# Kernel optimization log

Hardware: AMD Instinct MI355X
Metric: run time of the kernel (lower is better)

## Reference

```python
import jax, jax.numpy as jnp
import numpy as np

# Reconstructed laminar V1-V2 dynamics (submodule sources were not provided;
# dynamics follow the documented dependency order L4 -> PV -> V2 -> template -> SOM -> L2/3).
N = 36            # n_orientations
H = 128           # v2_hidden_dim
DT_TAU = 0.1      # dt/tau for rate units
DT_TAU_A = 0.02   # dt/tau for adaptation
BETA_A = 0.5      # adaptation strength
W_PV = 1.0        # PV (divisive-ish subtractive) inhibition weight
W_SOM = 0.8       # SOM inhibition weight
FB_GAIN = 0.5     # feedback center-excitation gain
ALPHA = 1.0       # error-signal template subtraction
FB_SCALE = 1.0    # feedback_scale buffer


def _ring_kernel(key, n, scale):
    return scale * jax.random.normal(key, (n, n), dtype=jnp.float32)


def setup_inputs() -> dict:
    key = jax.random.key(0)
    ks = jax.random.split(key, 16)
    B, T = 1024, 512
    D_in = 2 * N + 2  # 74 packed width
    s = 1.0 / np.sqrt(N)
    sh = 1.0 / np.sqrt(D_in + H)
    return {
        "packed_input": jax.random.normal(ks[0], (B, T, D_in), dtype=jnp.float32),
        "W_l4": _ring_kernel(ks[1], N, s),
        "W_l23": _ring_kernel(ks[2], N, s),
        "W_som": _ring_kernel(ks[3], N, s),
        "Wz": sh * jax.random.normal(ks[4], (D_in + H, H), dtype=jnp.float32),
        "Wr": sh * jax.random.normal(ks[5], (D_in + H, H), dtype=jnp.float32),
        "Wh": sh * jax.random.normal(ks[6], (D_in + H, H), dtype=jnp.float32),
        "bz": jnp.zeros((H,), jnp.float32),
        "br": jnp.zeros((H,), jnp.float32),
        "bh": jnp.zeros((H,), jnp.float32),
        "Wq": (1.0 / np.sqrt(H)) * jax.random.normal(ks[7], (H, N), dtype=jnp.float32),
        "bq": jnp.zeros((N,), jnp.float32),
        "Wp": (1.0 / np.sqrt(H)) * jax.random.normal(ks[8], (H, 1), dtype=jnp.float32),
        "bp": jnp.zeros((1,), jnp.float32),
        "Ws": (1.0 / np.sqrt(H)) * jax.random.normal(ks[9], (H, 3), dtype=jnp.float32),
        "bs": jnp.zeros((3,), jnp.float32),
    }


def _forward(packed_input, W_l4, W_l23, W_som, Wz, Wr, Wh, bz, br, bh,
             Wq, bq, Wp, bp, Ws, bs):
    B, T, _ = packed_input.shape
    stim_seq = packed_input[..., :N]          # [B,T,N]
    cue_seq = packed_input[..., N:2 * N]      # [B,T,N]
    task_seq = packed_input[..., 2 * N:]      # [B,T,2]

    def gru(x, h):
        xh = jnp.concatenate([x, h], axis=-1)
        z = jax.nn.sigmoid(xh @ Wz + bz)
        r = jax.nn.sigmoid(xh @ Wr + br)
        xrh = jnp.concatenate([x, r * h], axis=-1)
        hh = jnp.tanh(xrh @ Wh + bh)
        return (1.0 - z) * h + z * hh

    def step(state, inp):
        r_l4, r_l23, r_pv, r_som, adapt, h_v2 = state
        stimulus, cue, task_state = inp
        # --- V1 L4 ring (with adaptation, PV inhibition) ---
        drive_l4 = stimulus + r_l4 @ W_l4.T - W_PV * r_pv - adapt
        r_l4_n = r_l4 + DT_TAU * (-r_l4 + jax.nn.relu(drive_l4))
        adapt_n = adapt + DT_TAU_A * (-adapt + BETA_A * r_l4_n)
        # --- PV pool (single unit per batch) ---
        pv_in = jnp.mean(r_l4_n, axis=-1, keepdims=True) + jnp.mean(r_l23, axis=-1, keepdims=True)
        r_pv_n = r_pv + DT_TAU * (-r_pv + jax.nn.relu(pv_in))
        # --- V2 context module (uses r_l23 at t-1) ---
        v2_in = jnp.concatenate([r_l23, cue, task_state], axis=-1)  # [B,74]
        h_v2_n = gru(v2_in, h_v2)
        q_pred = jax.nn.softmax(h_v2_n @ Wq + bq, axis=-1)          # [B,N]
        pi_raw = jax.nn.sigmoid(h_v2_n @ Wp + bp)                   # [B,1]
        state_logits = h_v2_n @ Ws + bs                              # [B,3]
        pi_eff = pi_raw * FB_SCALE
        # --- deep template + feedback signals ---
        deep_tmpl = q_pred * pi_eff
        som_drive = q_pred * pi_eff
        r_som_n = r_som + DT_TAU * (-r_som + jax.nn.relu(som_drive + r_som @ W_som.T))
        tmpl_mod = 1.0 + FB_GAIN * q_pred * pi_eff
        l4_to_l23 = r_l4_n - ALPHA * deep_tmpl
        # --- V1 L2/3 ring ---
        drive_l23 = l4_to_l23 * tmpl_mod + r_l23 @ W_l23.T - W_SOM * r_som_n - W_PV * r_pv_n
        r_l23_n = r_l23 + DT_TAU * (-r_l23 + jax.nn.relu(drive_l23))
        new_state = (r_l4_n, r_l23_n, r_pv_n, r_som_n, adapt_n, h_v2_n)
        return new_state, r_l23_n

    z = jnp.zeros((B, N), jnp.float32)
    init = (z, z, jnp.zeros((B, 1), jnp.float32), z, z, jnp.zeros((B, H), jnp.float32))
    inputs = (jnp.swapaxes(stim_seq, 0, 1), jnp.swapaxes(cue_seq, 0, 1), jnp.swapaxes(task_seq, 0, 1))
    _, r_l23_all = jax.lax.scan(step, init, inputs)  # [T,B,N]
    return jnp.swapaxes(r_l23_all, 0, 1)             # [B,T,N]


def reference(packed_input, W_l4, W_l23, W_som, Wz, Wr, Wh, bz, br, bh,
              Wq, bq, Wp, bp, Ws, bs):
    return _forward(packed_input, W_l4, W_l23, W_som, Wz, Wr, Wh, bz, br, bh,
                    Wq, bq, Wp, bp, Ws, bs)
```

## Files before the change

### kernel.cpp

```cpp
#include <hip/hip_runtime.h>
#include <cstdint>
#include <cstddef>


#define NN   36
#define HH   128
#define DIN  74
#define KT   202
#define KP   232
#define TT   512
#define RPB  4
#define NPAD 40
#define HSTR 136
#define S2   6

typedef short bf16x8 __attribute__((ext_vector_type(8)));
typedef float f32x4  __attribute__((ext_vector_type(4)));

#define MFMA(a,b,c) __builtin_amdgcn_mfma_f32_16x16x32_bf16((a),(b),(c),0,0,0)
#define BAR() asm volatile("s_waitcnt lgkmcnt(0)\n\ts_barrier" ::: "memory")

__device__ __forceinline__ float fastrcp(float x) { return __builtin_amdgcn_rcpf(x); }
__device__ __forceinline__ float sigmf(float x) { return fastrcp(1.0f + __expf(-x)); }
__device__ __forceinline__ float tanhf_fast(float x) {
    return 1.0f - 2.0f * fastrcp(1.0f + __expf(2.0f * x));
}

__device__ __forceinline__ short f2bf(float v) {
    union { float f; unsigned u; } x; x.f = v;
    unsigned r = (x.u + 0x7fffu + ((x.u >> 16) & 1u)) >> 16;
    return (short)r;
}
__device__ __forceinline__ float bf2f(short s) {
    union { unsigned u; float f; } y; y.u = ((unsigned)(unsigned short)s) << 16;
    return y.f;
}

__device__ __forceinline__ unsigned cvtpk(float a, float b) {
    unsigned r;
    asm("v_cvt_pk_bf16_f32 %0, %1, %2" : "=v"(r) : "v"(a), "v"(b));
    return r;
}
__device__ __forceinline__ float lo16f(unsigned p) { return __uint_as_float(p << 16); }
__device__ __forceinline__ float hi16f(unsigned p) { return __uint_as_float(p & 0xffff0000u); }

#define DPP_STEP_MAX(x, ctrl) \
    x = fmaxf(x, __int_as_float(__builtin_amdgcn_update_dpp(0, __float_as_int(x), (ctrl), 0xF, 0xF, true)))
#define DPP_STEP_SUM(x, ctrl) \
    x = x + __int_as_float(__builtin_amdgcn_update_dpp(0, __float_as_int(x), (ctrl), 0xF, 0xF, true))

__device__ __forceinline__ float red16_max(float x) {
    DPP_STEP_MAX(x, 0xB1);
    DPP_STEP_MAX(x, 0x4E);
    DPP_STEP_MAX(x, 0x141);
    DPP_STEP_MAX(x, 0x140);
    return x;
}
__device__ __forceinline__ float red16_sum(float x) {
    DPP_STEP_SUM(x, 0xB1);
    DPP_STEP_SUM(x, 0x4E);
    DPP_STEP_SUM(x, 0x141);
    DPP_STEP_SUM(x, 0x140);
    return x;
}

#define HEADBASE 86016
#define FRAG_TOTAL 92160

extern "C" __global__ void __launch_bounds__(256)
init_frags(const float* __restrict__ Wz, const float* __restrict__ Wr,
           const float* __restrict__ Wh, const float* __restrict__ Wq,
           const float* __restrict__ Wp, short* __restrict__ frag)
{
    int idx = blockIdx.x * 256 + threadIdx.x;
    if (idx >= FRAG_TOTAL) return;
    float v;
    if (idx < HEADBASE) {
        int T = idx / 3584; int rem = idx - T * 3584;
        int s = rem >> 9;   int e = rem & 511;
        int l = e >> 3, j = e & 7;
        int k = s * 32 + ((l >> 4) << 3) + j;
        int n = ((T & 7) << 4) + (l & 15);
        const float* W = (T < 8) ? Wz : (T < 16) ? Wr : Wh;
        v = (k < KT) ? W[k * HH + n] : 0.f;
    } else {
        int r2 = idx - HEADBASE;
        int ts = r2 >> 9; int e = r2 & 511;
        int t = ts >> 2, s = ts & 3;
        int l = e >> 3, j = e & 7;
        int k = s * 32 + ((l >> 4) << 3) + j;
        int c = (t << 4) + (l & 15);
        v = (c < NN) ? Wq[k * NN + c] : (c == NN ? Wp[k] : 0.f);
    }
    frag[idx] = f2bf(v);
}

extern "C" __global__ void __launch_bounds__(1024, 4)
laminar_kernel(const float* __restrict__ packed,
               const float* __restrict__ Wl4,
               const float* __restrict__ Wl23,
               const float* __restrict__ Wsom,
               const float* __restrict__ bz,
               const float* __restrict__ br,
               const float* __restrict__ bh,
               const float* __restrict__ bq,
               const float* __restrict__ bp,
               const short* __restrict__ frag,
               float* __restrict__ out)
{
    const int tid  = threadIdx.x;
    const int r0   = blockIdx.x * RPB;
    const int lane = tid & 63;
    const int w    = tid >> 6;
    const int m    = lane & 15;
    const int q    = lane >> 4;
    const int arow = m & 7;
    const int ab   = arow >> 1;
    const int ap   = arow & 1;
    const int b0i  = (q & 1) << 1;
    const int b1i  = b0i + 1;

    __shared__ __align__(16) short xa[2][RPB][KP];
    __shared__ __align__(16) short xb[2][RPB][KP];
    __shared__ __align__(16) short hbS[2][RPB][HSTR];
    __shared__ float hS[HH][S2];
    __shared__ float zgS[HH][S2];
    __shared__ float preq[48][S2];
    __shared__ __align__(16) float W4l4[1296], W4l23[1296], W4som[1296];
    __shared__ __align__(16) float l4s[2][RPB][NPAD];
    __shared__ __align__(16) float l23s[RPB][NPAD];
    __shared__ __align__(16) float soms[RPB][NPAD], adL[RPB][NPAD];
    __shared__ __align__(16) float l4part[RPB][NPAD];
    __shared__ __align__(16) float l23dotS[RPB][NPAD];
    __shared__ __align__(16) float somdotS[RPB][NPAD];
    __shared__ float bzL[HH], brL[HH], bhL[HH], bqL[48];
    __shared__ float pvL[RPB];
    __shared__ float bpS;

    for (int i = tid; i < HH; i += 1024) { bzL[i] = bz[i]; brL[i] = br[i]; bhL[i] = bh[i]; }
    for (int i = tid; i < 48; i += 1024) bqL[i] = (i < NN) ? bq[i] : 0.f;
    if (tid == 0) bpS = bp[0];
    for (int idx = tid; idx < 324; idx += 1024) {
        const int c = idx / NN, i = idx - c * NN;
        const int o = idx * 4;
        #pragma unroll
        for (int d = 0; d < 4; ++d) {
            W4l4[o + d]  = Wl4[i * NN + 4 * c + d];
            W4l23[o + d] = Wl23[i * NN + 4 * c + d];
            W4som[o + d] = Wsom[i * NN + 4 * c + d];
        }
    }
    { short* p = (short*)xa;  for (int i = tid; i < 2*RPB*KP;   i += 1024) p[i] = 0; }
    { short* p = (short*)xb;  for (int i = tid; i < 2*RPB*KP;   i += 1024) p[i] = 0; }
    { short* p = (short*)hbS; for (int i = tid; i < 2*RPB*HSTR; i += 1024) p[i] = 0; }
    { float* p = (float*)hS;  for (int i = tid; i < HH*S2;      i += 1024) p[i] = 0.f; }
    { float* p = (float*)l4s; for (int i = tid; i < 2*RPB*NPAD; i += 1024) p[i] = 0.f; }
    { float* p = (float*)l23s; for (int i = tid; i < RPB*NPAD;  i += 1024) {
        p[i] = 0.f; ((float*)soms)[i] = 0.f; ((float*)adL)[i] = 0.f;
        ((float*)l23dotS)[i] = 0.f; ((float*)somdotS)[i] = 0.f; } }
    if (tid < RPB) pvL[tid] = 0.f;

    bf16x8 FA[7], FB[7];
    if (w < 8) {
        const short* a0 = frag + (w * 7) * 512 + lane * 8;
        const short* b0 = frag + ((8 + w) * 7) * 512 + lane * 8;
        #pragma unroll
        for (int s = 0; s < 7; ++s) {
            FA[s] = *(const bf16x8*)(a0 + s * 512);
            FB[s] = *(const bf16x8*)(b0 + s * 512);
        }
    } else {
        const int hw8 = w - 8;
        const short* a0 = frag + ((16 + hw8) * 7) * 512 + lane * 8;
        #pragma unroll
        for (int s = 0; s < 7; ++s) FA[s] = *(const bf16x8*)(a0 + s * 512);
        const int hw = (hw8 < 3) ? hw8 : 0;
        const short* b0 = frag + HEADBASE + (hw * 4) * 512 + lane * 8;
        #pragma unroll
        for (int s = 0; s < 4; ++s) FB[s] = *(const bf16x8*)(b0 + s * 512);
        FB[4] = FA[4]; FB[5] = FA[5]; FB[6] = FA[6];
    }

    const int  idA = (w - 13) * 64 + lane;
    const bool isDotA = (w >= 13) && (idA < 144);
    const int  vA = idA < 144 ? (idA < 0 ? 0 : idA) : 0;
    const int  drA = (isDotA ? vA : 0) / 36, diA = (isDotA ? vA : 0) - drA * 36;
    const float* dAW = W4l23 + diA * 4;
    const float* dAS = &l23s[drA][0];
    float*       dAD = &l23dotS[drA][diA];
    const int  idB = (w - 8) * 64 + lane;
    const bool isL4f = (w >= 8 && w < 11) && (idB < 144);
    const int  vB = isL4f ? idB : 0;
    const int  lr = vB / 36, li = vB - lr * 36;
    const int  idC = w * 64 + lane;
    const bool isDotC = (w < 3) && (idC < 144);
    const int  vC = isDotC ? idC : 0;
    const int  crC = vC / 36, ciC = vC - crC * 36;
    const float* dCW = W4som + ciC * 4;
    const float* dCS = &soms[crC][0];
    float*       dCD = &somdotS[crC][ciC];
    const int  idD = (w - 3) * 64 + lane;
    const bool isL4p = (w >= 3 && w < 6) && (idD < 144);
    const int  vD = isL4p ? idD : 0;
    const int  prD = vD / 36, piD = vD - prD * 36;
    const float* pW = W4l4 + piD * 4;
    const int  idE = (w - 6) * 64 + lane;
    const bool isCue = (w >= 6 && w < 8) && (idE < 76);
    const int  evE = isCue ? idE : 0;
    const int  ctr = evE / 19;
    const int  ctc = 36 + 2 * (evE - ctr * 19);

    __syncthreads();

    float ctv0 = 0.f, ctv1 = 0.f, stimreg = 0.f;
    if (tid < RPB * NN) {
        const int r = tid / NN, i = tid - (tid / NN) * NN;
        const size_t b = ((size_t)(r0 + r) * TT) * DIN + i;
        const float s0 = packed[b];
        const float nl4 = 0.1f * fmaxf(s0, 0.f);
        l4s[0][r][i] = nl4;
        const float ad = 0.01f * nl4;
        adL[r][i] = ad;
        l4part[r][i] = packed[b + DIN] - ad;
    }
    if (isL4f) stimreg = packed[((size_t)(r0 + lr) * TT + 2) * DIN + li];
    if (isCue) {
        const size_t base0 = ((size_t)(r0 + ctr) * TT + 0) * DIN;
        #pragma unroll
        for (int d = 0; d < 2; ++d) {
            const float v = packed[base0 + ctc + d];
            const short hi = f2bf(v), lo = f2bf(v - bf2f(hi));
            xa[0][ctr][ctc + d] = hi; xa[1][ctr][ctc + d] = lo;
            if (ctc + d >= 64) { xb[0][ctr][ctc + d] = hi; xb[1][ctr][ctc + d] = lo; }
        }
        const size_t base1 = ((size_t)(r0 + ctr) * TT + 1) * DIN;
        ctv0 = packed[base1 + ctc]; ctv1 = packed[base1 + ctc + 1];
    }
    __syncthreads();

    for (int t = 0; t < TT; ++t) {
        float (*l4cur)[NPAD] = l4s[t & 1];
        float (*l4nxt)[NPAD] = l4s[(t + 1) & 1];

        if (w < 8) {
            const short* xaRow = &xa[ap][ab][0];
            bf16x8 Ax[7];
            #pragma unroll
            for (int s = 0; s < 7; ++s)
                Ax[s] = *(const bf16x8*)&xaRow[s * 32 + q * 8];
            f32x4 az = {0.f,0.f,0.f,0.f}, ar = {0.f,0.f,0.f,0.f};
            #pragma unroll
            for (int s = 0; s < 7; ++s) {
                az = MFMA(Ax[s], FA[s], az);
                ar = MFMA(Ax[s], FB[s], ar);
            }
            if (lane < 32) {
                const int f = w * 16 + m;
                const float z0 = az[0] + az[1], z1 = az[2] + az[3];
                const float r0v = ar[0] + ar[1], r1v = ar[2] + ar[3];
                zgS[f][b0i] = z0 + bzL[f];
                zgS[f][b1i] = z1 + bzL[f];
                const float ra = sigmf(r0v + brL[f]) * hS[f][b0i];
                const float rb = sigmf(r1v + brL[f]) * hS[f][b1i];
                const unsigned ph = cvtpk(ra, rb);
                const unsigned pl = cvtpk(ra - lo16f(ph), rb - hi16f(ph));
                xb[0][b0i][DIN + f] = (short)ph;         xb[1][b0i][DIN + f] = (short)pl;
                xb[0][b1i][DIN + f] = (short)(ph >> 16); xb[1][b1i][DIN + f] = (short)(pl >> 16);
            }
        } else if (isDotA) {
            float acc = 0.f;
            #pragma unroll
            for (int c = 0; c < 9; ++c) {
                const float4 wv = *(const float4*)&dAW[c * 144];
                const float4 sv = *(const float4*)&dAS[4 * c];
                acc += sv.x*wv.x + sv.y*wv.y + sv.z*wv.z + sv.w*wv.w;
            }
            *dAD = acc;
        }
        BAR();

        if (w >= 8) {
            const short* xaRow = &xa[ap][ab][0];
            const short* xbRow = &xb[ap][ab][0];
            bf16x8 Op[7];
            Op[0] = *(const bf16x8*)&xaRow[q * 8];
            Op[1] = *(const bf16x8*)&xaRow[32 + q * 8];
            #pragma unroll
            for (int s = 2; s < 7; ++s)
                Op[s] = *(const bf16x8*)&xbRow[s * 32 + q * 8];
            f32x4 a = {0.f,0.f,0.f,0.f}, b = {0.f,0.f,0.f,0.f};
            a = MFMA(Op[0], FA[0], a);
            b = MFMA(Op[1], FA[1], b);
            a = MFMA(Op[2], FA[2], a);
            b = MFMA(Op[3], FA[3], b);
            a = MFMA(Op[4], FA[4], a);
            b = MFMA(Op[5], FA[5], b);
            a = MFMA(Op[6], FA[6], a);
            a = a + b;
            if (lane < 32) {
                const int f = (w - 8) * 16 + m;
                const float s0 = a[0] + a[1], s1 = a[2] + a[3];
                const float hh0 = tanhf_fast(s0 + bhL[f]);
                const float hh1 = tanhf_fast(s1 + bhL[f]);
                const float zg0 = sigmf(zgS[f][b0i]);
                const float zg1 = sigmf(zgS[f][b1i]);
                const float hn0 = (1.0f - zg0) * hS[f][b0i] + zg0 * hh0;
                const float hn1 = (1.0f - zg1) * hS[f][b1i] + zg1 * hh1;
                hS[f][b0i] = hn0; hS[f][b1i] = hn1;
                const unsigned ph = cvtpk(hn0, hn1);
                const unsigned pl = cvtpk(hn0 - lo16f(ph), hn1 - hi16f(ph));
                hbS[0][b0i][f] = (short)ph;         hbS[1][b0i][f] = (short)pl;
                hbS[0][b1i][f] = (short)(ph >> 16); hbS[1][b1i][f] = (short)(pl >> 16);
                xa[0][b0i][DIN + f] = (short)ph;         xa[1][b0i][DIN + f] = (short)pl;
                xa[0][b1i][DIN + f] = (short)(ph >> 16); xa[1][b1i][DIN + f] = (short)(pl >> 16);
            }
        } else if (isDotC) {
            float acc = 0.f;
            #pragma unroll
            for (int c = 0; c < 9; ++c) {
                const float4 wv = *(const float4*)&dCW[c * 144];
                const float4 sv = *(const float4*)&dCS[4 * c];
                acc += sv.x*wv.x + sv.y*wv.y + sv.z*wv.z + sv.w*wv.w;
            }
            *dCD = acc;
        } else if (w == 6) {
            const int row = q;
            float s = l4cur[row][m] + l23s[row][m] + l4cur[row][m + 16] + l23s[row][m + 16];
            if (m < 4) s += l4cur[row][m + 32] + l23s[row][m + 32];
            s = red16_sum(s);
            if (m == 0) pvL[row] = 0.9f * pvL[row] + 0.1f * fmaxf(s * (1.0f / 36.0f), 0.f);
        }
        BAR();

        if (w >= 8 && w < 11) {
            const short* hbRow = &hbS[ap][ab][0];
            bf16x8 Hk[4];
            #pragma unroll
            for (int s = 0; s < 4; ++s)
                Hk[s] = *(const bf16x8*)&hbRow[s * 32 + q * 8];
            f32x4 a = {0.f,0.f,0.f,0.f};
            #pragma unroll
            for (int s = 0; s < 4; ++s) a = MFMA(Hk[s], FB[s], a);
            if (lane < 32) {
                const int c = (w - 8) * 16 + m;
                preq[c][b0i] = a[0] + a[1];
                preq[c][b1i] = a[2] + a[3];
            }
        } else if (isL4p) {
            const float* pS = &l4cur[prD][0];
            float acc = l4part[prD][piD];
            #pragma unroll
            for (int c = 0; c < 9; ++c) {
                const float4 wv = *(const float4*)&pW[c * 144];
                const float4 sv = *(const float4*)&pS[4 * c];
                acc += sv.x*wv.x + sv.y*wv.y + sv.z*wv.z + sv.w*wv.w;
            }
            l4part[prD][piD] = acc;
        } else if (isCue) {
            const unsigned ph = cvtpk(ctv0, ctv1);
            const unsigned pl = cvtpk(ctv0 - lo16f(ph), ctv1 - hi16f(ph));
            xa[0][ctr][ctc]     = (short)ph;         xa[1][ctr][ctc]     = (short)pl;
            xa[0][ctr][ctc + 1] = (short)(ph >> 16); xa[1][ctr][ctc + 1] = (short)(pl >> 16);
            if (ctc >= 64) {
                xb[0][ctr][ctc]     = (short)ph;         xb[1][ctr][ctc]     = (short)pl;
                xb[0][ctr][ctc + 1] = (short)(ph >> 16); xb[1][ctr][ctc + 1] = (short)(pl >> 16);
            }
            const int tn = (t + 2 < TT) ? t + 2 : TT - 1;
            const size_t base = ((size_t)(r0 + ctr) * TT + tn) * DIN;
            ctv0 = packed[base + ctc]; ctv1 = packed[base + ctc + 1];
        }
        BAR();

        if (w < 4) {
            const int rr = w;
            const float v0 = preq[m][rr] + bqL[m];
            const float v1 = preq[m + 16][rr] + bqL[m + 16];
            const float v2 = (m < 4) ? (preq[m + 32][rr] + bqL[m + 32]) : -1e30f;
            const float pi = sigmf(preq[36][rr] + bpS);
            const float mx = red16_max(fmaxf(fmaxf(v0, v1), v2));
            const float e0 = __expf(v0 - mx);
            const float e1 = __expf(v1 - mx);
            const float e2 = (m < 4) ? __expf(v2 - mx) : 0.f;
            const float ss = red16_sum(e0 + e1 + e2);
            const float sc = fastrcp(ss) * pi;
            if (lane < 16) {
                const float pv = pvL[rr];
                const size_t outb = ((size_t)(r0 + rr) * TT + t) * NN;
                float ln01[2];
                #pragma unroll
                for (int t2 = 0; t2 < 2; ++t2) {
                    const int i = m + 16 * t2;
                    const float dt = (t2 ? e1 : e0) * sc;
                    const float sn = 0.9f * soms[rr][i]
                                   + 0.1f * fmaxf(dt + somdotS[rr][i], 0.f);
                    soms[rr][i] = sn;
                    const float acc2 = (l4cur[rr][i] - dt) * (1.0f + 0.5f * dt)
                                     + l23dotS[rr][i] - 0.8f * sn - pv;
                    const float ln = 0.9f * l23s[rr][i] + 0.1f * fmaxf(acc2, 0.f);
                    l23s[rr][i] = ln;
                    out[outb + i] = ln;
                    ln01[t2] = ln;
                }
                const unsigned ph = cvtpk(ln01[0], ln01[1]);
                const unsigned pl = cvtpk(ln01[0] - lo16f(ph), ln01[1] - hi16f(ph));
                xa[0][rr][m]      = (short)ph;         xa[1][rr][m]      = (short)pl;
                xa[0][rr][m + 16] = (short)(ph >> 16); xa[1][rr][m + 16] = (short)(pl >> 16);
                if (m < 4) {
                    const int i = m + 32;
                    const float dt = e2 * sc;
                    const float sn = 0.9f * soms[rr][i]
                                   + 0.1f * fmaxf(dt + somdotS[rr][i], 0.f);
                    soms[rr][i] = sn;
                    const float acc2 = (l4cur[rr][i] - dt) * (1.0f + 0.5f * dt)
                                     + l23dotS[rr][i] - 0.8f * sn - pv;
                    const float ln = 0.9f * l23s[rr][i] + 0.1f * fmaxf(acc2, 0.f);
                    l23s[rr][i] = ln;
                    out[outb + i] = ln;
                    const short hi2 = f2bf(ln);
                    xa[0][rr][i] = hi2; xa[1][rr][i] = f2bf(ln - bf2f(hi2));
                }
            }
        } else if (isL4f) {
            const float nl4 = 0.9f * l4cur[lr][li]
                            + 0.1f * fmaxf(l4part[lr][li] - pvL[lr], 0.f);
            l4nxt[lr][li] = nl4;
            const float ad = 0.98f * adL[lr][li] + 0.01f * nl4;
            adL[lr][li] = ad;
            l4part[lr][li] = stimreg - ad;
            const int tn = (t + 3 < TT) ? t + 3 : TT - 1;
            stimreg = packed[((size_t)(r0 + lr) * TT + tn) * DIN + li];
        }
        BAR();
    }
}

extern "C" void kernel_launch(void* const* d_in, const int* in_sizes, int n_in,
                              void* d_out, int out_size, void* d_ws, size_t ws_size,
                              hipStream_t stream) {
    (void)in_sizes; (void)n_in; (void)out_size; (void)ws_size;
    const float* packed = (const float*)d_in[0];
    const float* Wl4    = (const float*)d_in[1];
    const float* Wl23   = (const float*)d_in[2];
    const float* Wsom   = (const float*)d_in[3];
    const float* Wz     = (const float*)d_in[4];
    const float* Wr     = (const float*)d_in[5];
    const float* Wh     = (const float*)d_in[6];
    const float* bz     = (const float*)d_in[7];
    const float* br     = (const float*)d_in[8];
    const float* bh     = (const float*)d_in[9];
    const float* Wq     = (const float*)d_in[10];
    const float* bq     = (const float*)d_in[11];
    const float* Wp     = (const float*)d_in[12];
    const float* bp     = (const float*)d_in[13];
    float* out  = (float*)d_out;
    short* frag = (short*)d_ws;

    init_frags<<<(FRAG_TOTAL + 255) / 256, 256, 0, stream>>>(Wz, Wr, Wh, Wq, Wp, frag);
    laminar_kernel<<<256, 1024, 0, stream>>>(packed, Wl4, Wl23, Wsom,
                                             bz, br, bh, bq, bp, frag, out);
}
```

Before: 1.416 ms.

## Restructure per-step schedule from four barrier phases to three, merging head and L2/3 update

The per-timestep loop is reorganised so that a single wave (w==0) computes the readout-head MFMAs from head weights staged in shared memory and then immediately does the softmax and L2/3/SOM update. This removes the preq scratch buffer and one block-wide barrier per step. The L4 update and the two ring dot products are moved onto the otherwise idle GRU waves 8-15 in the first phase. The work is therefore reassigned across waves, and the L4 state pipeline is shifted by one step. The trade-off is a longer serial critical path inside wave 0, plus extra LDS used for the head weights.

```diff
diff --git a/kernel.cpp b/kernel.cpp
--- a/kernel.cpp
+++ b/kernel.cpp
@@ -123,9 +123,9 @@
     __shared__ __align__(16) short xa[2][RPB][KP];
     __shared__ __align__(16) short xb[2][RPB][KP];
     __shared__ __align__(16) short hbS[2][RPB][HSTR];
+    __shared__ __align__(16) short HdL[6144];
     __shared__ float hS[HH][S2];
     __shared__ float zgS[HH][S2];
-    __shared__ float preq[48][S2];
     __shared__ __align__(16) float W4l4[1296], W4l23[1296], W4som[1296];
     __shared__ __align__(16) float l4s[2][RPB][NPAD];
     __shared__ __align__(16) float l23s[RPB][NPAD];
@@ -150,6 +150,7 @@
             W4som[o + d] = Wsom[i * NN + 4 * c + d];
         }
     }
+    for (int i = tid; i < 6144; i += 1024) HdL[i] = frag[HEADBASE + i];
     { short* p = (short*)xa;  for (int i = tid; i < 2*RPB*KP;   i += 1024) p[i] = 0; }
     { short* p = (short*)xb;  for (int i = tid; i < 2*RPB*KP;   i += 1024) p[i] = 0; }
     { short* p = (short*)hbS; for (int i = tid; i < 2*RPB*HSTR; i += 1024) p[i] = 0; }
@@ -170,43 +171,31 @@
             FB[s] = *(const bf16x8*)(b0 + s * 512);
         }
     } else {
-        const int hw8 = w - 8;
-        const short* a0 = frag + ((16 + hw8) * 7) * 512 + lane * 8;
+        const short* a0 = frag + ((16 + (w - 8)) * 7) * 512 + lane * 8;
         #pragma unroll
-        for (int s = 0; s < 7; ++s) FA[s] = *(const bf16x8*)(a0 + s * 512);
-        const int hw = (hw8 < 3) ? hw8 : 0;
-        const short* b0 = frag + HEADBASE + (hw * 4) * 512 + lane * 8;
-        #pragma unroll
-        for (int s = 0; s < 4; ++s) FB[s] = *(const bf16x8*)(b0 + s * 512);
-        FB[4] = FA[4]; FB[5] = FA[5]; FB[6] = FA[6];
-    }
-
-    const int  idA = (w - 13) * 64 + lane;
-    const bool isDotA = (w >= 13) && (idA < 144);
-    const int  vA = idA < 144 ? (idA < 0 ? 0 : idA) : 0;
-    const int  drA = (isDotA ? vA : 0) / 36, diA = (isDotA ? vA : 0) - drA * 36;
+        for (int s = 0; s < 7; ++s) { FA[s] = *(const bf16x8*)(a0 + s * 512); FB[s] = FA[s]; }
+    }
+
+    const int  auxA = (w - 8) * 64 + lane;
+    const bool isL4f  = (w >= 8) && (auxA < 144);
+    const bool isDotA = (w >= 8) && (auxA >= 144) && (auxA < 288);
+    const bool isDotC = (w >= 8) && (auxA >= 288) && (auxA < 432);
+    const int  vB = isL4f ? auxA : 0;
+    const int  lr = vB / 36, li = vB - lr * 36;
+    const int  vA = isDotA ? (auxA - 144) : 0;
+    const int  drA = vA / 36, diA = vA - drA * 36;
     const float* dAW = W4l23 + diA * 4;
-    const float* dAS = &l23s[drA][0];
-    float*       dAD = &l23dotS[drA][diA];
-    const int  idB = (w - 8) * 64 + lane;
-    const bool isL4f = (w >= 8 && w < 11) && (idB < 144);
-    const int  vB = isL4f ? idB : 0;
-    const int  lr = vB / 36, li = vB - lr * 36;
-    const int  idC = w * 64 + lane;
-    const bool isDotC = (w < 3) && (idC < 144);
-    const int  vC = isDotC ? idC : 0;
+    const int  vC = isDotC ? (auxA - 288) : 0;
     const int  crC = vC / 36, ciC = vC - crC * 36;
     const float* dCW = W4som + ciC * 4;
-    const float* dCS = &soms[crC][0];
-    float*       dCD = &somdotS[crC][ciC];
-    const int  idD = (w - 3) * 64 + lane;
-    const bool isL4p = (w >= 3 && w < 6) && (idD < 144);
-    const int  vD = isL4p ? idD : 0;
+    const int  auxB = (w - 1) * 64 + lane;
+    const bool isL4p = (w >= 1 && w < 4) && (auxB < 144);
+    const int  vD = isL4p ? auxB : 0;
     const int  prD = vD / 36, piD = vD - prD * 36;
     const float* pW = W4l4 + piD * 4;
-    const int  idE = (w - 6) * 64 + lane;
-    const bool isCue = (w >= 6 && w < 8) && (idE < 76);
-    const int  evE = isCue ? idE : 0;
+    const int  auxC = (w - 1) * 64 + lane;
+    const bool isCue = (w >= 1 && w < 3) && (auxC < 76);
+    const int  evE = isCue ? auxC : 0;
     const int  ctr = evE / 19;
     const int  ctc = 36 + 2 * (evE - ctr * 19);
 
@@ -215,15 +204,9 @@
     float ctv0 = 0.f, ctv1 = 0.f, stimreg = 0.f;
     if (tid < RPB * NN) {
         const int r = tid / NN, i = tid - (tid / NN) * NN;
-        const size_t b = ((size_t)(r0 + r) * TT) * DIN + i;
-        const float s0 = packed[b];
-        const float nl4 = 0.1f * fmaxf(s0, 0.f);
-        l4s[0][r][i] = nl4;
-        const float ad = 0.01f * nl4;
-        adL[r][i] = ad;
-        l4part[r][i] = packed[b + DIN] - ad;
-    }
-    if (isL4f) stimreg = packed[((size_t)(r0 + lr) * TT + 2) * DIN + li];
+        l4part[r][i] = packed[((size_t)(r0 + r) * TT + 0) * DIN + i];
+    }
+    if (isL4f) stimreg = packed[((size_t)(r0 + lr) * TT + 1) * DIN + li];
     if (isCue) {
         const size_t base0 = ((size_t)(r0 + ctr) * TT + 0) * DIN;
         #pragma unroll
@@ -239,8 +222,8 @@
     __syncthreads();
 
     for (int t = 0; t < TT; ++t) {
-        float (*l4cur)[NPAD] = l4s[t & 1];
-        float (*l4nxt)[NPAD] = l4s[(t + 1) & 1];
+        float (*l4cur)[NPAD]  = l4s[t & 1];
+        float (*l4prev)[NPAD] = l4s[(t + 1) & 1];
 
         if (w < 8) {
             const short* xaRow = &xa[ap][ab][0];
@@ -267,15 +250,33 @@
                 xb[0][b0i][DIN + f] = (short)ph;         xb[1][b0i][DIN + f] = (short)pl;
                 xb[0][b1i][DIN + f] = (short)(ph >> 16); xb[1][b1i][DIN + f] = (short)(pl >> 16);
             }
+        } else if (isL4f) {
+            const float nl4 = 0.9f * l4prev[lr][li]
+                            + 0.1f * fmaxf(l4part[lr][li] - pvL[lr], 0.f);
+            l4cur[lr][li] = nl4;
+            const float ad = 0.98f * adL[lr][li] + 0.01f * nl4;
+            adL[lr][li] = ad;
+            l4part[lr][li] = stimreg - ad;
+            const int tn = (t + 2 < TT) ? t + 2 : TT - 1;
+            stimreg = packed[((size_t)(r0 + lr) * TT + tn) * DIN + li];
         } else if (isDotA) {
             float acc = 0.f;
             #pragma unroll
             for (int c = 0; c < 9; ++c) {
                 const float4 wv = *(const float4*)&dAW[c * 144];
-                const float4 sv = *(const float4*)&dAS[4 * c];
+                const float4 sv = *(const float4*)&l23s[drA][4 * c];
                 acc += sv.x*wv.x + sv.y*wv.y + sv.z*wv.z + sv.w*wv.w;
             }
-            *dAD = acc;
+            l23dotS[drA][diA] = acc;
+        } else if (isDotC) {
+            float acc = 0.f;
+            #pragma unroll
+            for (int c = 0; c < 9; ++c) {
+                const float4 wv = *(const float4*)&dCW[c * 144];
+                const float4 sv = *(const float4*)&soms[crC][4 * c];
+                acc += sv.x*wv.x + sv.y*wv.y + sv.z*wv.z + sv.w*wv.w;
+            }
+            somdotS[crC][ciC] = acc;
         }
         BAR();
 
@@ -314,38 +315,12 @@
                 xa[0][b0i][DIN + f] = (short)ph;         xa[1][b0i][DIN + f] = (short)pl;
                 xa[0][b1i][DIN + f] = (short)(ph >> 16); xa[1][b1i][DIN + f] = (short)(pl >> 16);
             }
-        } else if (isDotC) {
-            float acc = 0.f;
-            #pragma unroll
-            for (int c = 0; c < 9; ++c) {
-                const float4 wv = *(const float4*)&dCW[c * 144];
-                const float4 sv = *(const float4*)&dCS[4 * c];
-                acc += sv.x*wv.x + sv.y*wv.y + sv.z*wv.z + sv.w*wv.w;
-            }
-            *dCD = acc;
-        } else if (w == 6) {
+        } else if (w == 0) {
             const int row = q;
             float s = l4cur[row][m] + l23s[row][m] + l4cur[row][m + 16] + l23s[row][m + 16];
             if (m < 4) s += l4cur[row][m + 32] + l23s[row][m + 32];
             s = red16_sum(s);
             if (m == 0) pvL[row] = 0.9f * pvL[row] + 0.1f * fmaxf(s * (1.0f / 36.0f), 0.f);
-        }
-        BAR();
-
-        if (w >= 8 && w < 11) {
-            const short* hbRow = &hbS[ap][ab][0];
-            bf16x8 Hk[4];
-            #pragma unroll
-            for (int s = 0; s < 4; ++s)
-                Hk[s] = *(const bf16x8*)&hbRow[s * 32 + q * 8];
-            f32x4 a = {0.f,0.f,0.f,0.f};
-            #pragma unroll
-            for (int s = 0; s < 4; ++s) a = MFMA(Hk[s], FB[s], a);
-            if (lane < 32) {
-                const int c = (w - 8) * 16 + m;
-                preq[c][b0i] = a[0] + a[1];
-                preq[c][b1i] = a[2] + a[3];
-            }
         } else if (isL4p) {
             const float* pS = &l4cur[prD][0];
             float acc = l4part[prD][piD];
@@ -356,6 +331,77 @@
                 acc += sv.x*wv.x + sv.y*wv.y + sv.z*wv.z + sv.w*wv.w;
             }
             l4part[prD][piD] = acc;
+        }
+        BAR();
+
+        if (w == 0) {
+            const short* hbRow = &hbS[ap][ab][0];
+            bf16x8 Hk[4];
+            #pragma unroll
+            for (int s = 0; s < 4; ++s)
+                Hk[s] = *(const bf16x8*)&hbRow[s * 32 + q * 8];
+            f32x4 a0 = {0.f,0.f,0.f,0.f}, a1 = {0.f,0.f,0.f,0.f}, a2 = {0.f,0.f,0.f,0.f};
+            bf16x8 HdA[4], HdB[4];
+            #pragma unroll
+            for (int s = 0; s < 4; ++s) HdA[s] = *(const bf16x8*)&HdL[s * 512 + lane * 8];
+            #pragma unroll
+            for (int s = 0; s < 4; ++s) a0 = MFMA(Hk[s], HdA[s], a0);
+            #pragma unroll
+            for (int s = 0; s < 4; ++s) HdB[s] = *(const bf16x8*)&HdL[(4 + s) * 512 + lane * 8];
+            #pragma unroll
+            for (int s = 0; s < 4; ++s) a1 = MFMA(Hk[s], HdB[s], a1);
+            #pragma unroll
+            for (int s = 0; s < 4; ++s) HdA[s] = *(const bf16x8*)&HdL[(8 + s) * 512 + lane * 8];
+            #pragma unroll
+            for (int s = 0; s < 4; ++s) a2 = MFMA(Hk[s], HdA[s], a2);
+            const int  hsel = q >> 1;
+            const int  bat  = ((q & 1) << 1) | hsel;
+            const float v0  = (hsel ? (a0[2] + a0[3]) : (a0[0] + a0[1])) + bqL[m];
+            const float v1  = (hsel ? (a1[2] + a1[3]) : (a1[0] + a1[1])) + bqL[m + 16];
+            const float v2r =  hsel ? (a2[2] + a2[3]) : (a2[0] + a2[1]);
+            const float v2  = (m < 4) ? (v2r + bqL[m + 32]) : -1e30f;
+            const float pi  = sigmf(__shfl(v2r, (lane & 48) | 4) + bpS);
+            const float mx = red16_max(fmaxf(fmaxf(v0, v1), v2));
+            const float e0 = __expf(v0 - mx);
+            const float e1 = __expf(v1 - mx);
+            const float e2 = (m < 4) ? __expf(v2 - mx) : 0.f;
+            const float ss = red16_sum(e0 + e1 + e2);
+            const float sc = fastrcp(ss) * pi;
+            const float pv = pvL[bat];
+            const size_t outb = ((size_t)(r0 + bat) * TT + t) * NN;
+            float ln01[2];
+            #pragma unroll
+            for (int t2 = 0; t2 < 2; ++t2) {
+                const int i = m + 16 * t2;
+                const float dt = (t2 ? e1 : e0) * sc;
+                const float sn = 0.9f * soms[bat][i]
+                               + 0.1f * fmaxf(dt + somdotS[bat][i], 0.f);
+                soms[bat][i] = sn;
+                const float acc2 = (l4cur[bat][i] - dt) * (1.0f + 0.5f * dt)
+                                 + l23dotS[bat][i] - 0.8f * sn - pv;
+                const float ln = 0.9f * l23s[bat][i] + 0.1f * fmaxf(acc2, 0.f);
+                l23s[bat][i] = ln;
+                out[outb + i] = ln;
+                ln01[t2] = ln;
+            }
+            const unsigned ph = cvtpk(ln01[0], ln01[1]);
+            const unsigned pl = cvtpk(ln01[0] - lo16f(ph), ln01[1] - hi16f(ph));
+            xa[0][bat][m]      = (short)ph;         xa[1][bat][m]      = (short)pl;
+            xa[0][bat][m + 16] = (short)(ph >> 16); xa[1][bat][m + 16] = (short)(pl >> 16);
+            if (m < 4) {
+                const int i = m + 32;
+                const float dt = e2 * sc;
+                const float sn = 0.9f * soms[bat][i]
+                               + 0.1f * fmaxf(dt + somdotS[bat][i], 0.f);
+                soms[bat][i] = sn;
+                const float acc2 = (l4cur[bat][i] - dt) * (1.0f + 0.5f * dt)
+                                 + l23dotS[bat][i] - 0.8f * sn - pv;
+                const float ln = 0.9f * l23s[bat][i] + 0.1f * fmaxf(acc2, 0.f);
+                l23s[bat][i] = ln;
+                out[outb + i] = ln;
+                const short hi2 = f2bf(ln);
+                xa[0][bat][i] = hi2; xa[1][bat][i] = f2bf(ln - bf2f(hi2));
+            }
         } else if (isCue) {
             const unsigned ph = cvtpk(ctv0, ctv1);
             const unsigned pl = cvtpk(ctv0 - lo16f(ph), ctv1 - hi16f(ph));
@@ -368,67 +414,6 @@
             const int tn = (t + 2 < TT) ? t + 2 : TT - 1;
             const size_t base = ((size_t)(r0 + ctr) * TT + tn) * DIN;
             ctv0 = packed[base + ctc]; ctv1 = packed[base + ctc + 1];
-        }
-        BAR();
-
-        if (w < 4) {
-            const int rr = w;
-            const float v0 = preq[m][rr] + bqL[m];
-            const float v1 = preq[m + 16][rr] + bqL[m + 16];
-            const float v2 = (m < 4) ? (preq[m + 32][rr] + bqL[m + 32]) : -1e30f;
-            const float pi = sigmf(preq[36][rr] + bpS);
-            const float mx = red16_max(fmaxf(fmaxf(v0, v1), v2));
-            const float e0 = __expf(v0 - mx);
-            const float e1 = __expf(v1 - mx);
-            const float e2 = (m < 4) ? __expf(v2 - mx) : 0.f;
-            const float ss = red16_sum(e0 + e1 + e2);
-            const float sc = fastrcp(ss) * pi;
-            if (lane < 16) {
-                const float pv = pvL[rr];
-                const size_t outb = ((size_t)(r0 + rr) * TT + t) * NN;
-                float ln01[2];
-                #pragma unroll
-                for (int t2 = 0; t2 < 2; ++t2) {
-                    const int i = m + 16 * t2;
-                    const float dt = (t2 ? e1 : e0) * sc;
-                    const float sn = 0.9f * soms[rr][i]
-                                   + 0.1f * fmaxf(dt + somdotS[rr][i], 0.f);
-                    soms[rr][i] = sn;
-                    const float acc2 = (l4cur[rr][i] - dt) * (1.0f + 0.5f * dt)
-                                     + l23dotS[rr][i] - 0.8f * sn - pv;
-                    const float ln = 0.9f * l23s[rr][i] + 0.1f * fmaxf(acc2, 0.f);
-                    l23s[rr][i] = ln;
-                    out[outb + i] = ln;
-                    ln01[t2] = ln;
-                }
-                const unsigned ph = cvtpk(ln01[0], ln01[1]);
-                const unsigned pl = cvtpk(ln01[0] - lo16f(ph), ln01[1] - hi16f(ph));
-                xa[0][rr][m]      = (short)ph;         xa[1][rr][m]      = (short)pl;
-                xa[0][rr][m + 16] = (short)(ph >> 16); xa[1][rr][m + 16] = (short)(pl >> 16);
-                if (m < 4) {
-                    const int i = m + 32;
-                    const float dt = e2 * sc;
-                    const float sn = 0.9f * soms[rr][i]
-                                   + 0.1f * fmaxf(dt + somdotS[rr][i], 0.f);
-                    soms[rr][i] = sn;
-                    const float acc2 = (l4cur[rr][i] - dt) * (1.0f + 0.5f * dt)
-                                     + l23dotS[rr][i] - 0.8f * sn - pv;
-                    const float ln = 0.9f * l23s[rr][i] + 0.1f * fmaxf(acc2, 0.f);
-                    l23s[rr][i] = ln;
-                    out[outb + i] = ln;
-                    const short hi2 = f2bf(ln);
-                    xa[0][rr][i] = hi2; xa[1][rr][i] = f2bf(ln - bf2f(hi2));
-                }
-            }
-        } else if (isL4f) {
-            const float nl4 = 0.9f * l4cur[lr][li]
-                            + 0.1f * fmaxf(l4part[lr][li] - pvL[lr], 0.f);
-            l4nxt[lr][li] = nl4;
-            const float ad = 0.98f * adL[lr][li] + 0.01f * nl4;
-            adL[lr][li] = ad;
-            l4part[lr][li] = stimreg - ad;
-            const int tn = (t + 3 < TT) ? t + 3 : TT - 1;
-            stimreg = packed[((size_t)(r0 + lr) * TT + tn) * DIN + li];
         }
         BAR();
     }
```

New measurement: 1.654 ms. 16.8% more time.
